# Performance work log

Measured on AMD Instinct MI355X. Metric: run time of the kernel, lower is better.

## Reference

```python
import jax, jax.numpy as jnp
import numpy as np

B, N, D = 2048, 128, 32   # samples, features, per-feature embed dim
H = 8                     # num_head
ND = N * D                # flattened width = 4096
U = D * N // H            # per-head units = 512
DH = D // H               # per-head output feature dim = 4


def setup_inputs() -> dict:
    key = jax.random.key(0)
    k_x, k_q, k_k, k_v, k_o = jax.random.split(key, 5)
    scale_w = 0.02  # keep QK^T logits in a sane range for softmax
    x = jax.random.normal(k_x, (B, N, D), dtype=jnp.float32)
    Wq = jax.random.normal(k_q, (H, ND, U), dtype=jnp.float32) * scale_w
    Wk = jax.random.normal(k_k, (H, ND, U), dtype=jnp.float32) * scale_w
    Wv = jax.random.normal(k_v, (H, ND, U), dtype=jnp.float32) * scale_w
    Wo = jax.random.normal(k_o, (D, D), dtype=jnp.float32) * (1.0 / np.sqrt(D))
    return {"x": x, "Wq": Wq, "Wk": Wk, "Wv": Wv, "Wo": Wo}


def reference(x, Wq, Wk, Wv, Wo):
    b, n, d = x.shape
    scale = d ** (-0.5)          # note: original scales by feature dim d, not head dim
    xf = x.reshape(b, n * d)     # (b, nd); the leading 1 axis in TF is vacuous
    # Batched per-head projections (collapses the Python head loop into one GEMM each)
    q = jnp.einsum('bf,hfu->hbu', xf, Wq)   # (H, b, U)
    k = jnp.einsum('bf,hfu->hbu', xf, Wk)   # (H, b, U)
    v = jnp.einsum('bf,hfu->hbu', xf, Wv)   # (H, b, U)
    scores = jax.nn.softmax(jnp.einsum('hbu,hcu->hbc', q, k) * scale, axis=-1)  # (H, b, b)
    av = jnp.einsum('hbc,hcu->hbu', scores, v)              # (H, b, U)
    # per-head reshape (b, U) -> (b, n, d/H), then concat heads along last dim
    av = av.reshape(H, b, n, d // H)                         # (H, b, n, dh)
    concat = jnp.transpose(av, (1, 2, 0, 3)).reshape(b, n, d)  # (b, n, d)
    return concat @ Wo  # dropout rate is 0 -> identity
```

## Files before the change

kernel.cpp:

```cpp
#include <hip/hip_runtime.h>
#include <stdint.h>
#include <math.h>

typedef short    s16x8 __attribute__((ext_vector_type(8)));
typedef float    f32x4 __attribute__((ext_vector_type(4)));
typedef uint32_t u32x4 __attribute__((ext_vector_type(4)));
typedef unsigned short u16x4 __attribute__((ext_vector_type(4)));
typedef unsigned short u16x8 __attribute__((ext_vector_type(8)));

__device__ __forceinline__ uint16_t f2bf(float f) {
  union { float f; uint32_t u; } v; v.f = f;
  uint32_t r = v.u + 0x7fffu + ((v.u >> 16) & 1u);
  return (uint16_t)(r >> 16);
}
__device__ __forceinline__ float bf2f(uint16_t h) {
  union { uint32_t u; float f; } v; v.u = ((uint32_t)h) << 16;
  return v.f;
}

__device__ __forceinline__ void gld16(const void* g, void* l) {
  __builtin_amdgcn_global_load_lds(
      (const __attribute__((address_space(1))) void*)g,
      (__attribute__((address_space(3))) void*)l, 16, 0, 0);
}

__global__ __launch_bounds__(256) void cvt_x(const float* __restrict__ x,
                                             uint16_t* __restrict__ xf,
                                             float* __restrict__ rs) {
  if (blockIdx.x < 64) rs[blockIdx.x * 256 + threadIdx.x] = 0.f;
  size_t i = ((size_t)blockIdx.x * 256 + threadIdx.x) * 4;
  f32x4 v = *(const f32x4*)(x + i);
  u16x4 o = { f2bf(v.x), f2bf(v.y), f2bf(v.z), f2bf(v.w) };
  *(u16x4*)(xf + i) = o;
}

__global__ __launch_bounds__(256) void wtrans(const float* __restrict__ W0,
                                              const float* __restrict__ W1,
                                              const float* __restrict__ W2,
                                              uint16_t* __restrict__ Wt) {
  const int z = blockIdx.z;
  const float* W = (z < 8 ? W0 : (z < 16 ? W1 : W2)) + (size_t)(z & 7) * (4096 * 512);
  const int f0 = blockIdx.x * 64, u0 = blockIdx.y * 32;
  __shared__ float t[64][33];
  const int tid = threadIdx.x;
  {
    const int fi = tid >> 2, uu = (tid & 3) * 8;
    const float* src = W + (size_t)(f0 + fi) * 512 + u0 + uu;
    f32x4 v0 = *(const f32x4*)src;
    f32x4 v1 = *(const f32x4*)(src + 4);
    t[fi][uu] = v0.x; t[fi][uu + 1] = v0.y; t[fi][uu + 2] = v0.z; t[fi][uu + 3] = v0.w;
    t[fi][uu + 4] = v1.x; t[fi][uu + 5] = v1.y; t[fi][uu + 6] = v1.z; t[fi][uu + 7] = v1.w;
  }
  __syncthreads();
  {
    const int uo = tid >> 3, fo = (tid & 7) * 8;
    u16x8 o = { f2bf(t[fo][uo]),     f2bf(t[fo + 1][uo]), f2bf(t[fo + 2][uo]),
                f2bf(t[fo + 3][uo]), f2bf(t[fo + 4][uo]), f2bf(t[fo + 5][uo]),
                f2bf(t[fo + 6][uo]), f2bf(t[fo + 7][uo]) };
    *(u16x8*)&Wt[((size_t)z * 512 + u0 + uo) * 4096 + f0 + fo] = o;
  }
}

template <int MODE>
__global__ __launch_bounds__(256, 4) void gemm_bt(
    const uint16_t* __restrict__ A, size_t sAz,
    const uint16_t* __restrict__ B, size_t sBz,
    void* __restrict__ C0, void* __restrict__ C1,
    int K, float scale, float* __restrict__ rs) {
  const int tid = threadIdx.x;
  const int wave = tid >> 6, lane = tid & 63;
  const int quad = lane >> 4, l16 = lane & 15;
  const int wrow = (wave >> 1) * 64, wcol = (wave & 1) * 64;
  const int m0 = blockIdx.y * 128, n0 = blockIdx.x * 128;
  int z = blockIdx.z, kh = 0, Kloop = K;
  if (MODE == 3) { kh = z >> 3; z &= 7; Kloop = K >> 1; }
  A += (size_t)z * sAz + (size_t)kh * Kloop;
  B += (size_t)z * sBz + (size_t)kh * Kloop;

  __shared__ __align__(16) uint16_t lA[128 * 64];
  __shared__ __align__(16) uint16_t lB[128 * 64];

  f32x4 acc[4][4];
#pragma unroll
  for (int i = 0; i < 4; i++)
#pragma unroll
    for (int j = 0; j < 4; j++) acc[i][j] = f32x4{0.f, 0.f, 0.f, 0.f};

  const int lrow = lane >> 3;
  const int cs = ((lane & 7) ^ (lrow & 7)) * 8;
  const int rs0 = wave * 8;
  const uint16_t* gA = A + (size_t)(m0 + rs0 + lrow) * K + cs;
  const uint16_t* gB = B + (size_t)(n0 + rs0 + lrow) * K + cs;
  const size_t row32 = (size_t)32 * K;
  uint16_t* sA = &lA[rs0 * 64];
  uint16_t* sB = &lB[rs0 * 64];

  for (int k0 = 0; k0 < Kloop; k0 += 64) {
    __syncthreads();
#pragma unroll
    for (int g = 0; g < 4; g++) {
      gld16(gA + g * row32, sA + g * 2048);
      gld16(gB + g * row32, sB + g * 2048);
    }
    gA += 64; gB += 64;
    __syncthreads();
#pragma unroll
    for (int h = 0; h < 2; h++) {
      s16x8 af[4], bfr[4];
      const int fsw = (((h * 4 + quad) ^ (l16 & 7)) * 8);
#pragma unroll
      for (int i = 0; i < 4; i++)
        af[i] = *(const s16x8*)&lA[(wrow + i * 16 + l16) * 64 + fsw];
#pragma unroll
      for (int j = 0; j < 4; j++)
        bfr[j] = *(const s16x8*)&lB[(wcol + j * 16 + l16) * 64 + fsw];
#pragma unroll
      for (int i = 0; i < 4; i++)
#pragma unroll
        for (int j = 0; j < 4; j++)
          acc[i][j] = __builtin_amdgcn_mfma_f32_16x16x32_bf16(af[i], bfr[j], acc[i][j], 0, 0, 0);
    }
  }

  const int mb = m0 + wrow + quad * 4;
  const int nb = n0 + wcol + l16;
  if (MODE == 4) {
    if (z < 16) {
      uint16_t* C = (uint16_t*)C0 + ((size_t)z << 20);
#pragma unroll
      for (int i = 0; i < 4; i++)
#pragma unroll
        for (int j = 0; j < 4; j++)
#pragma unroll
          for (int r = 0; r < 4; r++)
            C[(size_t)(mb + i * 16 + r) * 512 + (nb + j * 16)] = f2bf(acc[i][j][r]);
    } else {
      uint16_t* C = (uint16_t*)C1 + ((size_t)(z - 16) << 20);
#pragma unroll
      for (int i = 0; i < 4; i++)
#pragma unroll
        for (int j = 0; j < 4; j++) {
          u16x4 o = { f2bf(acc[i][j][0]), f2bf(acc[i][j][1]),
                      f2bf(acc[i][j][2]), f2bf(acc[i][j][3]) };
          *(u16x4*)&C[(size_t)(nb + j * 16) * 2048 + (mb + i * 16)] = o;
        }
    }
  } else if (MODE == 2) {
    uint16_t* C = (uint16_t*)C0 + ((size_t)z << 22);
    float* rz = rs + (z << 11);
    float si[4][4];
#pragma unroll
    for (int i = 0; i < 4; i++)
#pragma unroll
      for (int r = 0; r < 4; r++) si[i][r] = 0.f;
#pragma unroll
    for (int i = 0; i < 4; i++)
#pragma unroll
      for (int j = 0; j < 4; j++)
#pragma unroll
        for (int r = 0; r < 4; r++) {
          float e = exp2f(fmaf(acc[i][j][r], scale, -43.2808512f));
          uint16_t hb = f2bf(e);
          C[(size_t)(mb + i * 16 + r) * 2048 + (nb + j * 16)] = hb;
          si[i][r] += bf2f(hb);
        }
#pragma unroll
    for (int i = 0; i < 4; i++)
#pragma unroll
      for (int r = 0; r < 4; r++) {
        float s = si[i][r];
        s += __shfl_xor(s, 1);
        s += __shfl_xor(s, 2);
        s += __shfl_xor(s, 4);
        s += __shfl_xor(s, 8);
        si[i][r] = s;
      }
    if (l16 == 0) {
#pragma unroll
      for (int i = 0; i < 4; i++)
#pragma unroll
        for (int r = 0; r < 4; r++)
          atomicAdd(&rz[mb + i * 16 + r], si[i][r]);
    }
  } else {
    float* C = (float*)(kh ? C1 : C0) + ((size_t)z << 20);
    const float* rz = rs + (z << 11);
#pragma unroll
    for (int i = 0; i < 4; i++)
#pragma unroll
      for (int r = 0; r < 4; r++) {
        float w = 1.0f / rz[mb + i * 16 + r];
#pragma unroll
        for (int j = 0; j < 4; j++)
          C[(size_t)(mb + i * 16 + r) * 512 + (nb + j * 16)] = acc[i][j][r] * w;
      }
  }
}

__global__ __launch_bounds__(256) void out_proj(const float* __restrict__ av0,
                                                const float* __restrict__ av1,
                                                const float* __restrict__ Wo,
                                                float* __restrict__ out) {
  __shared__ float lw[1024];
  const int tid = threadIdx.x;
#pragma unroll
  for (int i = 0; i < 4; i++) lw[tid + i * 256] = Wo[tid + i * 256];
  __syncthreads();
  const int p = blockIdx.x * 256 + tid;
  const int b = p >> 7, n = p & 127;
  float c[32];
#pragma unroll
  for (int hh = 0; hh < 8; hh++) {
    size_t idx = ((size_t)hh * 2048 + b) * 512 + n * 4;
    f32x4 v = *(const f32x4*)(av0 + idx);
    f32x4 w = *(const f32x4*)(av1 + idx);
    c[hh * 4] = v.x + w.x; c[hh * 4 + 1] = v.y + w.y;
    c[hh * 4 + 2] = v.z + w.z; c[hh * 4 + 3] = v.w + w.w;
  }
  float o[32];
#pragma unroll
  for (int d = 0; d < 32; d++) o[d] = 0.f;
#pragma unroll
  for (int j = 0; j < 32; j++) {
    float cj = c[j];
#pragma unroll
    for (int d = 0; d < 32; d++) o[d] = fmaf(cj, lw[j * 32 + d], o[d]);
  }
  float* dst = out + (size_t)p * 32;
#pragma unroll
  for (int i = 0; i < 8; i++) {
    f32x4 v = { o[i * 4], o[i * 4 + 1], o[i * 4 + 2], o[i * 4 + 3] };
    *(f32x4*)(dst + i * 4) = v;
  }
}

extern "C" void kernel_launch(void* const* d_in, const int* in_sizes, int n_in,
                              void* d_out, int out_size, void* d_ws, size_t ws_size,
                              hipStream_t stream) {
  const float* x  = (const float*)d_in[0];
  const float* Wq = (const float*)d_in[1];
  const float* Wk = (const float*)d_in[2];
  const float* Wv = (const float*)d_in[3];
  const float* Wo = (const float*)d_in[4];
  float* out = (float*)d_out;

  uint8_t* ws = (uint8_t*)d_ws;
  uint16_t* Wt  = (uint16_t*)(ws);
  uint16_t* P   = (uint16_t*)(ws);
  float*    av0 = (float*)(ws + 67108864);
  uint16_t* xf  = (uint16_t*)(ws + 100663296);
  uint16_t* q   = (uint16_t*)(ws + 117440512);
  float*    av1 = (float*)(ws + 117440512);
  uint16_t* vt  = (uint16_t*)(ws + 150994944);
  float*    rs  = (float*)(ws + 167772160);

  const size_t WtH = (size_t)512 * 4096;
  const float scale2 = 0.17677669529663687f * 1.4426950408889634f;

  cvt_x<<<8192, 256, 0, stream>>>(x, xf, rs);
  wtrans<<<dim3(64, 16, 24), 256, 0, stream>>>(Wq, Wk, Wv, Wt);

  gemm_bt<4><<<dim3(4, 16, 24), 256, 0, stream>>>(
      xf, 0, Wt, WtH, q, vt, 4096, 0.f, nullptr);

  gemm_bt<2><<<dim3(16, 16, 8), 256, 0, stream>>>(
      q, (size_t)2048 * 512, q + (size_t)8 * 2048 * 512, (size_t)2048 * 512,
      P, nullptr, 512, scale2, rs);

  gemm_bt<3><<<dim3(4, 16, 16), 256, 0, stream>>>(
      P, (size_t)2048 * 2048, vt, (size_t)512 * 2048,
      av0, av1, 2048, 0.f, rs);

  out_proj<<<1024, 256, 0, stream>>>(av0, av1, Wo, out);
}
```

Before: 575.3 us.

## Triple-buffer GEMM LDS loads and enlarge block tile to 256x128 with 8 waves

Reworks the shared bf16 GEMM kernel to use 512-thread blocks covering a 256x128 output tile, and replaces the load-then-compute loop with a three-stage LDS ring buffer. Async global-to-LDS loads for future K tiles are issued ahead, and explicit vmcnt waits let compute overlap memory latency. The goal is to hide global load latency and get more reuse of the B tile per block. In exchange LDS use grows to about 144 KB per block, which limits occupancy. The hand-counted vmcnt values depend on the exact number of loads issued per stage.

```diff
diff --git a/kernel.cpp b/kernel.cpp
--- a/kernel.cpp
+++ b/kernel.cpp
@@ -62,7 +62,7 @@
 }
 
 template <int MODE>
-__global__ __launch_bounds__(256, 4) void gemm_bt(
+__global__ __launch_bounds__(512, 2) void gemm_bt(
     const uint16_t* __restrict__ A, size_t sAz,
     const uint16_t* __restrict__ B, size_t sBz,
     void* __restrict__ C0, void* __restrict__ C1,
@@ -71,14 +71,14 @@
   const int wave = tid >> 6, lane = tid & 63;
   const int quad = lane >> 4, l16 = lane & 15;
   const int wrow = (wave >> 1) * 64, wcol = (wave & 1) * 64;
-  const int m0 = blockIdx.y * 128, n0 = blockIdx.x * 128;
+  const int m0 = blockIdx.y * 256, n0 = blockIdx.x * 128;
   int z = blockIdx.z, kh = 0, Kloop = K;
   if (MODE == 3) { kh = z >> 3; z &= 7; Kloop = K >> 1; }
   A += (size_t)z * sAz + (size_t)kh * Kloop;
   B += (size_t)z * sBz + (size_t)kh * Kloop;
 
-  __shared__ __align__(16) uint16_t lA[128 * 64];
-  __shared__ __align__(16) uint16_t lB[128 * 64];
+  __shared__ __align__(16) uint16_t lA[3 * 256 * 64];
+  __shared__ __align__(16) uint16_t lB[3 * 128 * 64];
 
   f32x4 acc[4][4];
 #pragma unroll
@@ -91,35 +91,65 @@
   const int rs0 = wave * 8;
   const uint16_t* gA = A + (size_t)(m0 + rs0 + lrow) * K + cs;
   const uint16_t* gB = B + (size_t)(n0 + rs0 + lrow) * K + cs;
-  const size_t row32 = (size_t)32 * K;
+  const size_t row64 = (size_t)64 * K;
   uint16_t* sA = &lA[rs0 * 64];
   uint16_t* sB = &lB[rs0 * 64];
 
-  for (int k0 = 0; k0 < Kloop; k0 += 64) {
-    __syncthreads();
-#pragma unroll
-    for (int g = 0; g < 4; g++) {
-      gld16(gA + g * row32, sA + g * 2048);
-      gld16(gB + g * row32, sB + g * 2048);
-    }
-    gA += 64; gB += 64;
-    __syncthreads();
+  const int nt = Kloop >> 6;
+
+  auto stage = [&](int t, int buf) {
+    const uint16_t* ga = gA + (size_t)t * 64;
+    const uint16_t* gb = gB + (size_t)t * 64;
+    uint16_t* sa = sA + buf * (256 * 64);
+    uint16_t* sb = sB + buf * (128 * 64);
+#pragma unroll
+    for (int g = 0; g < 4; g++)
+      gld16(ga + g * row64, sa + g * 4096);
+#pragma unroll
+    for (int g = 0; g < 2; g++)
+      gld16(gb + g * row64, sb + g * 4096);
+  };
+
+  auto compute = [&](int buf) {
+    const uint16_t* la = &lA[buf * (256 * 64)];
+    const uint16_t* lb = &lB[buf * (128 * 64)];
 #pragma unroll
     for (int h = 0; h < 2; h++) {
       s16x8 af[4], bfr[4];
       const int fsw = (((h * 4 + quad) ^ (l16 & 7)) * 8);
 #pragma unroll
       for (int i = 0; i < 4; i++)
-        af[i] = *(const s16x8*)&lA[(wrow + i * 16 + l16) * 64 + fsw];
+        af[i] = *(const s16x8*)&la[(wrow + i * 16 + l16) * 64 + fsw];
 #pragma unroll
       for (int j = 0; j < 4; j++)
-        bfr[j] = *(const s16x8*)&lB[(wcol + j * 16 + l16) * 64 + fsw];
+        bfr[j] = *(const s16x8*)&lb[(wcol + j * 16 + l16) * 64 + fsw];
 #pragma unroll
       for (int i = 0; i < 4; i++)
 #pragma unroll
         for (int j = 0; j < 4; j++)
           acc[i][j] = __builtin_amdgcn_mfma_f32_16x16x32_bf16(af[i], bfr[j], acc[i][j], 0, 0, 0);
     }
+  };
+
+  stage(0, 0);
+  stage(1, 1);
+  stage(2, 2);
+  asm volatile("s_waitcnt vmcnt(12)" ::: "memory");
+  __builtin_amdgcn_s_barrier();
+
+  for (int t = 0;; ++t) {
+    compute(t % 3);
+    if (t == nt - 1) break;
+    __builtin_amdgcn_s_barrier();
+    if (t + 3 < nt) {
+      stage(t + 3, t % 3);
+      asm volatile("s_waitcnt vmcnt(12)" ::: "memory");
+    } else if (t + 3 == nt) {
+      asm volatile("s_waitcnt vmcnt(6)" ::: "memory");
+    } else {
+      asm volatile("s_waitcnt vmcnt(0)" ::: "memory");
+    }
+    __builtin_amdgcn_s_barrier();
   }
 
   const int mb = m0 + wrow + quad * 4;
@@ -260,14 +290,14 @@
   cvt_x<<<8192, 256, 0, stream>>>(x, xf, rs);
   wtrans<<<dim3(64, 16, 24), 256, 0, stream>>>(Wq, Wk, Wv, Wt);
 
-  gemm_bt<4><<<dim3(4, 16, 24), 256, 0, stream>>>(
+  gemm_bt<4><<<dim3(4, 8, 24), 512, 0, stream>>>(
       xf, 0, Wt, WtH, q, vt, 4096, 0.f, nullptr);
 
-  gemm_bt<2><<<dim3(16, 16, 8), 256, 0, stream>>>(
+  gemm_bt<2><<<dim3(16, 8, 8), 512, 0, stream>>>(
       q, (size_t)2048 * 512, q + (size_t)8 * 2048 * 512, (size_t)2048 * 512,
       P, nullptr, 512, scale2, rs);
 
-  gemm_bt<3><<<dim3(4, 16, 16), 256, 0, stream>>>(
+  gemm_bt<3><<<dim3(4, 8, 16), 512, 0, stream>>>(
       P, (size_t)2048 * 2048, vt, (size_t)512 * 2048,
       av0, av1, 2048, 0.f, rs);
 
```

New measurement: 644.9 us. 1.12x slower.

## Rewrite GEMM as 256x256-tile, 8-wave, double-buffered pipelined MFMA kernel

Applied to the files above, without the earlier changes.

Replaces the 128x128 single-buffered GEMM with a 256x256 tile per 512-thread block. Each k step issues async global-to-LDS loads into a second 128KB LDS buffer, interleaved with MFMA quadrants and raised wave priority, so global latency overlaps compute. This roughly halves global traffic per FLOP and hides load latency. In exchange it cuts the grid size by four, uses 128KB of LDS per block so fewer blocks fit per CU, and relies on hand-placed barriers and waitcnts being correct.

```diff
diff --git a/kernel.cpp b/kernel.cpp
--- a/kernel.cpp
+++ b/kernel.cpp
@@ -62,7 +62,7 @@
 }
 
 template <int MODE>
-__global__ __launch_bounds__(256, 4) void gemm_bt(
+__global__ __launch_bounds__(512, 2) void gemm_bt(
     const uint16_t* __restrict__ A, size_t sAz,
     const uint16_t* __restrict__ B, size_t sBz,
     void* __restrict__ C0, void* __restrict__ C1,
@@ -70,65 +70,123 @@
   const int tid = threadIdx.x;
   const int wave = tid >> 6, lane = tid & 63;
   const int quad = lane >> 4, l16 = lane & 15;
-  const int wrow = (wave >> 1) * 64, wcol = (wave & 1) * 64;
-  const int m0 = blockIdx.y * 128, n0 = blockIdx.x * 128;
+  const int wm = wave >> 2, wn = wave & 3;
+  const int wnh = wn >> 1, wnl = wn & 1;
+  const int m0 = blockIdx.y * 256, n0 = blockIdx.x * 256;
   int z = blockIdx.z, kh = 0, Kloop = K;
   if (MODE == 3) { kh = z >> 3; z &= 7; Kloop = K >> 1; }
   A += (size_t)z * sAz + (size_t)kh * Kloop;
   B += (size_t)z * sBz + (size_t)kh * Kloop;
 
-  __shared__ __align__(16) uint16_t lA[128 * 64];
-  __shared__ __align__(16) uint16_t lB[128 * 64];
-
-  f32x4 acc[4][4];
-#pragma unroll
-  for (int i = 0; i < 4; i++)
+  __shared__ __align__(16) uint16_t lds[65536];
+
+  f32x4 acc[8][4];
+#pragma unroll
+  for (int i = 0; i < 8; i++)
 #pragma unroll
     for (int j = 0; j < 4; j++) acc[i][j] = f32x4{0.f, 0.f, 0.f, 0.f};
+  s16x8 af[4][2], bq0[2][2], bq1[2][2];
 
   const int lrow = lane >> 3;
   const int cs = ((lane & 7) ^ (lrow & 7)) * 8;
-  const int rs0 = wave * 8;
-  const uint16_t* gA = A + (size_t)(m0 + rs0 + lrow) * K + cs;
-  const uint16_t* gB = B + (size_t)(n0 + rs0 + lrow) * K + cs;
-  const size_t row32 = (size_t)32 * K;
-  uint16_t* sA = &lA[rs0 * 64];
-  uint16_t* sB = &lB[rs0 * 64];
-
-  for (int k0 = 0; k0 < Kloop; k0 += 64) {
-    __syncthreads();
-#pragma unroll
-    for (int g = 0; g < 4; g++) {
-      gld16(gA + g * row32, sA + g * 2048);
-      gld16(gB + g * row32, sB + g * 2048);
-    }
-    gA += 64; gB += 64;
-    __syncthreads();
-#pragma unroll
-    for (int h = 0; h < 2; h++) {
-      s16x8 af[4], bfr[4];
-      const int fsw = (((h * 4 + quad) ^ (l16 & 7)) * 8);
-#pragma unroll
-      for (int i = 0; i < 4; i++)
-        af[i] = *(const s16x8*)&lA[(wrow + i * 16 + l16) * 64 + fsw];
-#pragma unroll
-      for (int j = 0; j < 4; j++)
-        bfr[j] = *(const s16x8*)&lB[(wcol + j * 16 + l16) * 64 + fsw];
-#pragma unroll
-      for (int i = 0; i < 4; i++)
-#pragma unroll
-        for (int j = 0; j < 4; j++)
-          acc[i][j] = __builtin_amdgcn_mfma_f32_16x16x32_bf16(af[i], bfr[j], acc[i][j], 0, 0, 0);
-    }
-  }
-
-  const int mb = m0 + wrow + quad * 4;
-  const int nb = n0 + wcol + l16;
+  const uint16_t* gA = A + (size_t)(m0 + wave * 8 + lrow) * K + cs;
+  const uint16_t* gB = B + (size_t)(n0 + wave * 8 + lrow) * K + cs;
+  const size_t rs64 = (size_t)64 * K;
+  const int stW = wave * 512;
+
+#define STAGE(buf, mat, half, t)                                               \
+  do {                                                                         \
+    const uint16_t* gsrc =                                                     \
+        ((mat) ? gB : gA) + (size_t)(half) * 128 * K + (size_t)(t) * 64;       \
+    uint16_t* sdst =                                                           \
+        &lds[(buf) * 32768 + (mat) * 16384 + (half) * 8192 + stW];             \
+    gld16(gsrc, sdst);                                                         \
+    gld16(gsrc + rs64, sdst + 4096);                                           \
+  } while (0)
+
+#define LOAD_A(buf, ih)                                                        \
+  do {                                                                         \
+    const uint16_t* ba = &lds[(buf) * 32768 + wm * 8192];                      \
+    _Pragma("unroll") for (int i_ = 0; i_ < 4; i_++)                           \
+      _Pragma("unroll") for (int k_ = 0; k_ < 2; k_++)                         \
+        af[i_][k_] = *(const s16x8*)&ba[((ih) * 64 + i_ * 16 + l16) * 64 +     \
+                                        ((k_ * 4 + quad) ^ (l16 & 7)) * 8];    \
+  } while (0)
+
+#define LOAD_B(buf, jh, bq)                                                    \
+  do {                                                                         \
+    const uint16_t* bb = &lds[(buf) * 32768 + 16384 + wnh * 8192];             \
+    _Pragma("unroll") for (int j_ = 0; j_ < 2; j_++)                           \
+      _Pragma("unroll") for (int k_ = 0; k_ < 2; k_++)                         \
+        bq[j_][k_] = *(const s16x8*)&bb[(wnl * 64 + (jh) * 32 + j_ * 16 + l16) \
+                                            * 64 +                             \
+                                        ((k_ * 4 + quad) ^ (l16 & 7)) * 8];    \
+  } while (0)
+
+#define MMQ(ih, jh, bq)                                                        \
+  do {                                                                         \
+    __builtin_amdgcn_s_setprio(1);                                             \
+    _Pragma("unroll") for (int i_ = 0; i_ < 4; i_++)                           \
+      _Pragma("unroll") for (int j_ = 0; j_ < 2; j_++)                         \
+        _Pragma("unroll") for (int k_ = 0; k_ < 2; k_++)                       \
+          acc[(ih) * 4 + i_][(jh) * 2 + j_] =                                  \
+              __builtin_amdgcn_mfma_f32_16x16x32_bf16(                         \
+                  af[i_][k_], bq[j_][k_],                                      \
+                  acc[(ih) * 4 + i_][(jh) * 2 + j_], 0, 0, 0);                 \
+    __builtin_amdgcn_s_setprio(0);                                             \
+  } while (0)
+
+#define BAR __builtin_amdgcn_s_barrier()
+#define LGKM0 asm volatile("s_waitcnt lgkmcnt(0)" ::: "memory")
+#define VMW(n) asm volatile("s_waitcnt vmcnt(" #n ")" ::: "memory")
+
+  STAGE(0, 1, 0, 0); STAGE(0, 1, 1, 0);
+  STAGE(0, 0, 0, 0); STAGE(0, 0, 1, 0);
+  STAGE(1, 1, 0, 1); STAGE(1, 1, 1, 1);
+  VMW(4); BAR;
+
+  const int L = (Kloop >> 7) - 1;
+  for (int it = 0; it < L; ++it) {
+    const int t1 = 2 * it + 1, t2 = 2 * it + 2, t3 = 2 * it + 3;
+    LOAD_A(0, 0); LOAD_B(0, 0, bq0); STAGE(1, 0, 0, t1);
+    BAR; LGKM0; MMQ(0, 0, bq0); BAR;
+    LOAD_B(0, 1, bq1); STAGE(1, 0, 1, t1);
+    BAR; LGKM0; MMQ(0, 1, bq1); BAR;
+    LOAD_A(0, 1); STAGE(0, 1, 0, t2);
+    BAR; LGKM0; MMQ(1, 0, bq0); BAR;
+    STAGE(0, 1, 1, t2);
+    BAR; LGKM0; MMQ(1, 1, bq1); VMW(4); BAR;
+    LOAD_A(1, 0); LOAD_B(1, 0, bq0); STAGE(0, 0, 0, t2);
+    BAR; LGKM0; MMQ(0, 0, bq0); BAR;
+    LOAD_B(1, 1, bq1); STAGE(0, 0, 1, t2);
+    BAR; LGKM0; MMQ(0, 1, bq1); BAR;
+    LOAD_A(1, 1); STAGE(1, 1, 0, t3);
+    BAR; LGKM0; MMQ(1, 0, bq0); BAR;
+    STAGE(1, 1, 1, t3);
+    BAR; LGKM0; MMQ(1, 1, bq1); VMW(4); BAR;
+  }
+  {
+    const int t1 = 2 * L + 1;
+    LOAD_A(0, 0); LOAD_B(0, 0, bq0); STAGE(1, 0, 0, t1);
+    BAR; LGKM0; MMQ(0, 0, bq0); BAR;
+    LOAD_B(0, 1, bq1); STAGE(1, 0, 1, t1);
+    BAR; LGKM0; MMQ(0, 1, bq1); BAR;
+    LOAD_A(0, 1);
+    BAR; LGKM0; MMQ(1, 0, bq0); BAR;
+    MMQ(1, 1, bq1); VMW(0); BAR;
+    LOAD_A(1, 0); LOAD_B(1, 0, bq0); LGKM0; MMQ(0, 0, bq0);
+    LOAD_B(1, 1, bq1); LGKM0; MMQ(0, 1, bq1);
+    LOAD_A(1, 1); LGKM0; MMQ(1, 0, bq0);
+    MMQ(1, 1, bq1);
+  }
+
+  const int mb = m0 + wm * 128 + quad * 4;
+  const int nb = n0 + wn * 64 + l16;
   if (MODE == 4) {
     if (z < 16) {
       uint16_t* C = (uint16_t*)C0 + ((size_t)z << 20);
 #pragma unroll
-      for (int i = 0; i < 4; i++)
+      for (int i = 0; i < 8; i++)
 #pragma unroll
         for (int j = 0; j < 4; j++)
 #pragma unroll
@@ -137,7 +195,7 @@
     } else {
       uint16_t* C = (uint16_t*)C1 + ((size_t)(z - 16) << 20);
 #pragma unroll
-      for (int i = 0; i < 4; i++)
+      for (int i = 0; i < 8; i++)
 #pragma unroll
         for (int j = 0; j < 4; j++) {
           u16x4 o = { f2bf(acc[i][j][0]), f2bf(acc[i][j][1]),
@@ -148,13 +206,13 @@
   } else if (MODE == 2) {
     uint16_t* C = (uint16_t*)C0 + ((size_t)z << 22);
     float* rz = rs + (z << 11);
-    float si[4][4];
-#pragma unroll
-    for (int i = 0; i < 4; i++)
+    float si[8][4];
+#pragma unroll
+    for (int i = 0; i < 8; i++)
 #pragma unroll
       for (int r = 0; r < 4; r++) si[i][r] = 0.f;
 #pragma unroll
-    for (int i = 0; i < 4; i++)
+    for (int i = 0; i < 8; i++)
 #pragma unroll
       for (int j = 0; j < 4; j++)
 #pragma unroll
@@ -165,7 +223,7 @@
           si[i][r] += bf2f(hb);
         }
 #pragma unroll
-    for (int i = 0; i < 4; i++)
+    for (int i = 0; i < 8; i++)
 #pragma unroll
       for (int r = 0; r < 4; r++) {
         float s = si[i][r];
@@ -177,7 +235,7 @@
       }
     if (l16 == 0) {
 #pragma unroll
-      for (int i = 0; i < 4; i++)
+      for (int i = 0; i < 8; i++)
 #pragma unroll
         for (int r = 0; r < 4; r++)
           atomicAdd(&rz[mb + i * 16 + r], si[i][r]);
@@ -186,7 +244,7 @@
     float* C = (float*)(kh ? C1 : C0) + ((size_t)z << 20);
     const float* rz = rs + (z << 11);
 #pragma unroll
-    for (int i = 0; i < 4; i++)
+    for (int i = 0; i < 8; i++)
 #pragma unroll
       for (int r = 0; r < 4; r++) {
         float w = 1.0f / rz[mb + i * 16 + r];
@@ -195,6 +253,13 @@
           C[(size_t)(mb + i * 16 + r) * 512 + (nb + j * 16)] = acc[i][j][r] * w;
       }
   }
+#undef STAGE
+#undef LOAD_A
+#undef LOAD_B
+#undef MMQ
+#undef BAR
+#undef LGKM0
+#undef VMW
 }
 
 __global__ __launch_bounds__(256) void out_proj(const float* __restrict__ av0,
@@ -260,14 +325,14 @@
   cvt_x<<<8192, 256, 0, stream>>>(x, xf, rs);
   wtrans<<<dim3(64, 16, 24), 256, 0, stream>>>(Wq, Wk, Wv, Wt);
 
-  gemm_bt<4><<<dim3(4, 16, 24), 256, 0, stream>>>(
+  gemm_bt<4><<<dim3(2, 8, 24), 512, 0, stream>>>(
       xf, 0, Wt, WtH, q, vt, 4096, 0.f, nullptr);
 
-  gemm_bt<2><<<dim3(16, 16, 8), 256, 0, stream>>>(
+  gemm_bt<2><<<dim3(8, 8, 8), 512, 0, stream>>>(
       q, (size_t)2048 * 512, q + (size_t)8 * 2048 * 512, (size_t)2048 * 512,
       P, nullptr, 512, scale2, rs);
 
-  gemm_bt<3><<<dim3(4, 16, 16), 256, 0, stream>>>(
+  gemm_bt<3><<<dim3(2, 8, 16), 512, 0, stream>>>(
       P, (size_t)2048 * 2048, vt, (size_t)512 * 2048,
       av0, av1, 2048, 0.f, rs);
 
```

Result: faster. 550.1 us (-4.4%).

## Triple-buffer GEMM K-loop with 512-thread 128x256 tiles and split staging

Applied to the files above, without the earlier changes.

Rewrites the shared bf16 GEMM kernel to use 512-thread blocks computing 128x256 output tiles, with a three-stage LDS ring buffer fed by global_load_lds. Staging of the next-next tile is split between the two half-K sub-steps so loads overlap MFMA work, using explicit vmcnt/lgkmcnt waits, raw s_barrier, and s_setprio around the MFMA bursts. The aim is to hide global-load latency and reuse the A tile across more columns. In exchange it uses much more LDS per block (about 144 KB) and halves the grid, which lowers occupancy and block count per launch.

```diff
diff --git a/kernel.cpp b/kernel.cpp
--- a/kernel.cpp
+++ b/kernel.cpp
@@ -62,7 +62,7 @@
 }
 
 template <int MODE>
-__global__ __launch_bounds__(256, 4) void gemm_bt(
+__global__ __launch_bounds__(512, 2) void gemm_bt(
     const uint16_t* __restrict__ A, size_t sAz,
     const uint16_t* __restrict__ B, size_t sBz,
     void* __restrict__ C0, void* __restrict__ C1,
@@ -70,60 +70,99 @@
   const int tid = threadIdx.x;
   const int wave = tid >> 6, lane = tid & 63;
   const int quad = lane >> 4, l16 = lane & 15;
-  const int wrow = (wave >> 1) * 64, wcol = (wave & 1) * 64;
-  const int m0 = blockIdx.y * 128, n0 = blockIdx.x * 128;
+  const int wm = wave >> 2, wn = wave & 3;
+  const int m0 = blockIdx.y * 128, n0 = blockIdx.x * 256;
   int z = blockIdx.z, kh = 0, Kloop = K;
   if (MODE == 3) { kh = z >> 3; z &= 7; Kloop = K >> 1; }
   A += (size_t)z * sAz + (size_t)kh * Kloop;
   B += (size_t)z * sBz + (size_t)kh * Kloop;
 
-  __shared__ __align__(16) uint16_t lA[128 * 64];
-  __shared__ __align__(16) uint16_t lB[128 * 64];
+  __shared__ __align__(16) uint16_t lds[3 * 24576];
 
   f32x4 acc[4][4];
 #pragma unroll
   for (int i = 0; i < 4; i++)
 #pragma unroll
     for (int j = 0; j < 4; j++) acc[i][j] = f32x4{0.f, 0.f, 0.f, 0.f};
+  s16x8 af[4], bq[4];
 
   const int lrow = lane >> 3;
   const int cs = ((lane & 7) ^ (lrow & 7)) * 8;
-  const int rs0 = wave * 8;
-  const uint16_t* gA = A + (size_t)(m0 + rs0 + lrow) * K + cs;
-  const uint16_t* gB = B + (size_t)(n0 + rs0 + lrow) * K + cs;
-  const size_t row32 = (size_t)32 * K;
-  uint16_t* sA = &lA[rs0 * 64];
-  uint16_t* sB = &lB[rs0 * 64];
-
-  for (int k0 = 0; k0 < Kloop; k0 += 64) {
-    __syncthreads();
-#pragma unroll
-    for (int g = 0; g < 4; g++) {
-      gld16(gA + g * row32, sA + g * 2048);
-      gld16(gB + g * row32, sB + g * 2048);
-    }
-    gA += 64; gB += 64;
-    __syncthreads();
-#pragma unroll
-    for (int h = 0; h < 2; h++) {
-      s16x8 af[4], bfr[4];
-      const int fsw = (((h * 4 + quad) ^ (l16 & 7)) * 8);
-#pragma unroll
-      for (int i = 0; i < 4; i++)
-        af[i] = *(const s16x8*)&lA[(wrow + i * 16 + l16) * 64 + fsw];
-#pragma unroll
-      for (int j = 0; j < 4; j++)
-        bfr[j] = *(const s16x8*)&lB[(wcol + j * 16 + l16) * 64 + fsw];
-#pragma unroll
-      for (int i = 0; i < 4; i++)
-#pragma unroll
-        for (int j = 0; j < 4; j++)
-          acc[i][j] = __builtin_amdgcn_mfma_f32_16x16x32_bf16(af[i], bfr[j], acc[i][j], 0, 0, 0);
-    }
-  }
-
-  const int mb = m0 + wrow + quad * 4;
-  const int nb = n0 + wcol + l16;
+  const uint16_t* gA = A + (size_t)(m0 + wave * 8 + lrow) * K + cs;
+  const uint16_t* gB = B + (size_t)(n0 + wave * 8 + lrow) * K + cs;
+  const size_t rs64 = (size_t)64 * K;
+  const int stW = wave * 512;
+
+#define STAGE_A(t, buf)                                                        \
+  do {                                                                         \
+    const uint16_t* ga_ = gA + (size_t)(t) * 64;                               \
+    uint16_t* sa_ = &lds[(buf) * 24576 + stW];                                 \
+    gld16(ga_, sa_);                                                           \
+    gld16(ga_ + rs64, sa_ + 4096);                                             \
+  } while (0)
+
+#define STAGE_B01(t, buf)                                                      \
+  do {                                                                         \
+    const uint16_t* gb_ = gB + (size_t)(t) * 64;                               \
+    uint16_t* sb_ = &lds[(buf) * 24576 + 8192 + stW];                          \
+    gld16(gb_, sb_);                                                           \
+    gld16(gb_ + rs64, sb_ + 4096);                                             \
+  } while (0)
+
+#define STAGE_B23(t, buf)                                                      \
+  do {                                                                         \
+    const uint16_t* gb_ = gB + 2 * rs64 + (size_t)(t) * 64;                    \
+    uint16_t* sb_ = &lds[(buf) * 24576 + 8192 + 8192 + stW];                   \
+    gld16(gb_, sb_);                                                           \
+    gld16(gb_ + rs64, sb_ + 4096);                                             \
+  } while (0)
+
+#define LOAD_AB(buf, k_)                                                       \
+  do {                                                                         \
+    const uint16_t* ba_ = &lds[(buf) * 24576];                                 \
+    const int sw_ = (((k_) * 4 + quad) ^ (l16 & 7)) * 8;                       \
+    _Pragma("unroll") for (int i_ = 0; i_ < 4; i_++)                           \
+      af[i_] = *(const s16x8*)&ba_[(wm * 64 + i_ * 16 + l16) * 64 + sw_];      \
+    _Pragma("unroll") for (int j_ = 0; j_ < 4; j_++)                           \
+      bq[j_] = *(const s16x8*)&ba_[8192 + (wn * 64 + j_ * 16 + l16) * 64 + sw_];\
+  } while (0)
+
+#define MMQ                                                                    \
+  do {                                                                         \
+    __builtin_amdgcn_s_setprio(1);                                             \
+    _Pragma("unroll") for (int i_ = 0; i_ < 4; i_++)                           \
+      _Pragma("unroll") for (int j_ = 0; j_ < 4; j_++)                         \
+        acc[i_][j_] = __builtin_amdgcn_mfma_f32_16x16x32_bf16(                 \
+            af[i_], bq[j_], acc[i_][j_], 0, 0, 0);                             \
+    __builtin_amdgcn_s_setprio(0);                                             \
+  } while (0)
+
+#define BAR __builtin_amdgcn_s_barrier()
+#define LGKM0 asm volatile("s_waitcnt lgkmcnt(0)" ::: "memory")
+#define VMW(n) asm volatile("s_waitcnt vmcnt(" #n ")" ::: "memory")
+
+  const int nt = Kloop >> 6;
+
+  STAGE_A(0, 0); STAGE_B01(0, 0); STAGE_B23(0, 0);
+  STAGE_A(1, 1); STAGE_B01(1, 1); STAGE_B23(1, 1);
+  VMW(6); BAR;
+
+  for (int t = 0;; ++t) {
+    const int buf = t % 3, sbuf = (t + 2) % 3;
+    const bool st = (t + 2) < nt;
+    LOAD_AB(buf, 0);
+    if (st) { STAGE_A(t + 2, sbuf); STAGE_B01(t + 2, sbuf); }
+    BAR; LGKM0; MMQ; BAR;
+    LOAD_AB(buf, 1);
+    if (st) { STAGE_B23(t + 2, sbuf); }
+    BAR; LGKM0; MMQ;
+    if (t == nt - 1) break;
+    if (st) { VMW(6); } else if (t + 2 == nt) { VMW(0); }
+    BAR;
+  }
+
+  const int mb = m0 + wm * 64 + quad * 4;
+  const int nb = n0 + wn * 64 + l16;
   if (MODE == 4) {
     if (z < 16) {
       uint16_t* C = (uint16_t*)C0 + ((size_t)z << 20);
@@ -195,6 +234,14 @@
           C[(size_t)(mb + i * 16 + r) * 512 + (nb + j * 16)] = acc[i][j][r] * w;
       }
   }
+#undef STAGE_A
+#undef STAGE_B01
+#undef STAGE_B23
+#undef LOAD_AB
+#undef MMQ
+#undef BAR
+#undef LGKM0
+#undef VMW
 }
 
 __global__ __launch_bounds__(256) void out_proj(const float* __restrict__ av0,
@@ -260,14 +307,14 @@
   cvt_x<<<8192, 256, 0, stream>>>(x, xf, rs);
   wtrans<<<dim3(64, 16, 24), 256, 0, stream>>>(Wq, Wk, Wv, Wt);
 
-  gemm_bt<4><<<dim3(4, 16, 24), 256, 0, stream>>>(
+  gemm_bt<4><<<dim3(2, 16, 24), 512, 0, stream>>>(
       xf, 0, Wt, WtH, q, vt, 4096, 0.f, nullptr);
 
-  gemm_bt<2><<<dim3(16, 16, 8), 256, 0, stream>>>(
+  gemm_bt<2><<<dim3(8, 16, 8), 512, 0, stream>>>(
       q, (size_t)2048 * 512, q + (size_t)8 * 2048 * 512, (size_t)2048 * 512,
       P, nullptr, 512, scale2, rs);
 
-  gemm_bt<3><<<dim3(4, 16, 16), 256, 0, stream>>>(
+  gemm_bt<3><<<dim3(2, 16, 16), 512, 0, stream>>>(
       P, (size_t)2048 * 2048, vt, (size_t)512 * 2048,
       av0, av1, 2048, 0.f, rs);
 
```

Measured after the change: 574.4 us. No clear change (-0.1%).
